# Kernel optimization log

Measured on AMD Instinct MI355X. Metric: run time of the kernel, lower is better.

The kernel has to match this reference:

```python
import jax, jax.numpy as jnp
import numpy as np

N = 100000   # nodes
E = 800000   # directed edges (before self-loops)
D = 256      # in_feats == out_feats


def setup_inputs() -> dict:
    key = jax.random.key(0)
    ks = jax.random.split(key, 6)
    scale = 1.0 / np.sqrt(D)
    features = jax.random.normal(ks[0], (N, D), dtype=jnp.float32)
    src = jax.random.randint(ks[1], (E,), 0, N, dtype=jnp.int32)
    dst = jax.random.randint(ks[2], (E,), 0, N, dtype=jnp.int32)
    W1 = jax.random.normal(ks[3], (D, D), dtype=jnp.float32) * scale
    b1 = jnp.zeros((D,), dtype=jnp.float32)
    W2 = jax.random.normal(ks[4], (D, D), dtype=jnp.float32) * scale
    b2 = jnp.zeros((D,), dtype=jnp.float32)
    return {"features": features, "src": src, "dst": dst,
            "W1": W1, "b1": b1, "W2": W2, "b2": b2}


def _graph_conv(h, src, dst, norm_src, norm_dst, W, b):
    # DGL GraphConv, norm='both': out = D_in^{-1/2} A (D_out^{-1/2} h W) + b
    h = (h * norm_src) @ W            # [N, D] project (W first; in==out)
    agg = jax.ops.segment_sum(h[src], dst, num_segments=N)  # SpMM gather-scatter
    return agg * norm_dst + b


def reference(features, src, dst, W1, b1, W2, b2):
    # forward does g = dgl.add_self_loop(g)
    loops = jnp.arange(N, dtype=src.dtype)
    s = jnp.concatenate([src, loops])
    d = jnp.concatenate([dst, loops])
    ones = jnp.ones_like(s, dtype=jnp.float32)
    deg_out = jax.ops.segment_sum(ones, s, num_segments=N)   # out-degree (src side)
    deg_in = jax.ops.segment_sum(ones, d, num_segments=N)    # in-degree  (dst side)
    norm_src = jnp.where(deg_out > 0, deg_out ** -0.5, 0.0)[:, None]
    norm_dst = jnp.where(deg_in > 0, deg_in ** -0.5, 0.0)[:, None]
    x = _graph_conv(features, s, d, norm_src, norm_dst, W1, b1)
    x = jax.nn.relu(x)
    x = _graph_conv(x, s, d, norm_src, norm_dst, W2, b2)
    return x
```

## Files before the change

### kernel.cpp

```cpp
#include <hip/hip_runtime.h>

#define NN 100000
#define DD 256
#define SCAN_BLK 1024

typedef unsigned int uint;
typedef unsigned short ushort;
typedef __attribute__((ext_vector_type(8))) short bfx8;
typedef __attribute__((ext_vector_type(4))) float fx4;

__device__ __forceinline__ ushort f2bf(float f) {
    uint u = __float_as_uint(f);
    u += 0x7fff + ((u >> 16) & 1);
    return (ushort)(u >> 16);
}

__global__ __launch_bounds__(256) void k_init_deg(int* __restrict__ dego,
                                                  int* __restrict__ degi) {
    int i = blockIdx.x * 256 + threadIdx.x;
    if (i < NN) { dego[i] = 1; degi[i] = 1; }
}

__global__ __launch_bounds__(256) void k_count(const int* __restrict__ src,
                                               const int* __restrict__ dst, int E,
                                               int* __restrict__ dego,
                                               int* __restrict__ degi) {
    int e = blockIdx.x * 256 + threadIdx.x;
    if (e < E) {
        atomicAdd(&dego[src[e]], 1);
        atomicAdd(&degi[dst[e]], 1);
    }
}

__global__ __launch_bounds__(256) void k_norm(const int* __restrict__ dego,
                                              const int* __restrict__ degi,
                                              float* __restrict__ ns,
                                              float* __restrict__ nd) {
    int i = blockIdx.x * 256 + threadIdx.x;
    if (i < NN) {
        ns[i] = rsqrtf((float)dego[i]);
        nd[i] = rsqrtf((float)degi[i]);
    }
}

__device__ __forceinline__ int block_scan_inc(int v, int* sm) {
    int t = threadIdx.x;
    sm[t] = v;
    __syncthreads();
    for (int o = 1; o < SCAN_BLK; o <<= 1) {
        int x = (t >= o) ? sm[t - o] : 0;
        __syncthreads();
        sm[t] += x;
        __syncthreads();
    }
    return sm[t];
}

__global__ __launch_bounds__(SCAN_BLK) void k_scan1(const int* __restrict__ degi,
                                                    int* __restrict__ partials) {
    __shared__ int sm[SCAN_BLK];
    int i = blockIdx.x * SCAN_BLK + threadIdx.x;
    int v = (i < NN) ? (degi[i] - 1) : 0;
    block_scan_inc(v, sm);
    if (threadIdx.x == 0) partials[blockIdx.x] = sm[SCAN_BLK - 1];
}

__global__ __launch_bounds__(128) void k_scan2(int* __restrict__ partials, int nb) {
    __shared__ int sm[128];
    int t = threadIdx.x;
    int v = (t < nb) ? partials[t] : 0;
    sm[t] = v;
    __syncthreads();
    for (int o = 1; o < 128; o <<= 1) {
        int x = (t >= o) ? sm[t - o] : 0;
        __syncthreads();
        sm[t] += x;
        __syncthreads();
    }
    if (t < nb) partials[t] = sm[t] - v;
}

__global__ __launch_bounds__(SCAN_BLK) void k_scan3(const int* __restrict__ degi,
                                                    const int* __restrict__ partials,
                                                    int* __restrict__ rowptr,
                                                    int* __restrict__ cursor) {
    __shared__ int sm[SCAN_BLK];
    int i = blockIdx.x * SCAN_BLK + threadIdx.x;
    int v = (i < NN) ? (degi[i] - 1) : 0;
    int incl = block_scan_inc(v, sm);
    int excl = partials[blockIdx.x] + incl - v;
    if (i <= NN) rowptr[i] = excl;
    if (i < NN) cursor[i] = excl;
}

__global__ __launch_bounds__(256) void k_fill(const int* __restrict__ src,
                                              const int* __restrict__ dst, int E,
                                              int* __restrict__ cursor,
                                              int* __restrict__ eidx) {
    int e = blockIdx.x * 256 + threadIdx.x;
    if (e < E) {
        int d = dst[e];
        int p = atomicAdd(&cursor[d], 1);
        eidx[p] = src[e];
    }
}

__global__ __launch_bounds__(256) void k_convW(const float* __restrict__ W,
                                               ushort* __restrict__ Wt) {
    int n = blockIdx.x, k = threadIdx.x;
    Wt[n * DD + k] = f2bf(W[(size_t)k * DD + n]);
}

template <bool FP32A>
__global__ __launch_bounds__(512, 4) void k_mfgemm(const void* __restrict__ Av,
                                                   const float* __restrict__ nrm,
                                                   const ushort* __restrict__ Wt,
                                                   ushort* __restrict__ H) {
    __shared__ uint4 atq[2][128 * 8];
    int t = threadIdx.x;
    int brow = blockIdx.x * 128;
    int lane = t & 63, w = t >> 6;
    int wr = w >> 2, wc = w & 3;
    int lg = lane >> 4, lr = lane & 15;

    int sr = t >> 3, sc = t & 7;
    int rows_[2];
    float ns_[2];
#pragma unroll
    for (int i = 0; i < 2; ++i) {
        int r = brow + sr + i * 64;
        if (r >= NN) r = NN - 1;
        rows_[i] = r;
        if (FP32A) ns_[i] = nrm[r];
    }

    const uint4* wb[4];
#pragma unroll
    for (int ni = 0; ni < 4; ++ni)
        wb[ni] = (const uint4*)(Wt + (size_t)(wc * 64 + ni * 16 + lr) * DD);

    fx4 acc[4][4];
#pragma unroll
    for (int mi = 0; mi < 4; ++mi)
#pragma unroll
        for (int ni = 0; ni < 4; ++ni)
            acc[mi][ni] = (fx4){0.f, 0.f, 0.f, 0.f};

    uint4 sva[2];
    float4 svf[2][2];

    auto ldA = [&](int ks) {
        if (FP32A) {
            const float* X = (const float*)Av;
#pragma unroll
            for (int i = 0; i < 2; ++i) {
                const float4* p =
                    (const float4*)(X + (size_t)rows_[i] * DD + ks * 64 + sc * 8);
                svf[i][0] = p[0];
                svf[i][1] = p[1];
            }
        } else {
            const ushort* A = (const ushort*)Av;
#pragma unroll
            for (int i = 0; i < 2; ++i)
                sva[i] = *(const uint4*)(A + (size_t)rows_[i] * DD + ks * 64 + sc * 8);
        }
    };
    auto wrA = [&](int buf) {
#pragma unroll
        for (int i = 0; i < 2; ++i) {
            int r = sr + i * 64;
            uint4 u;
            if (FP32A) {
                float s = ns_[i];
                float4 a = svf[i][0], b = svf[i][1];
                u.x = (uint)f2bf(a.x * s) | ((uint)f2bf(a.y * s) << 16);
                u.y = (uint)f2bf(a.z * s) | ((uint)f2bf(a.w * s) << 16);
                u.z = (uint)f2bf(b.x * s) | ((uint)f2bf(b.y * s) << 16);
                u.w = (uint)f2bf(b.z * s) | ((uint)f2bf(b.w * s) << 16);
            } else {
                u = sva[i];
            }
            atq[buf][r * 8 + (sc ^ (r & 7))] = u;
        }
    };

    ldA(0);
    wrA(0);
    __syncthreads();

    int buf = 0;
#pragma unroll
    for (int ks = 0; ks < 4; ++ks) {
        if (ks < 3) ldA(ks + 1);
#pragma unroll
        for (int kk = 0; kk < 2; ++kk) {
            bfx8 bfr[4], af[4];
#pragma unroll
            for (int ni = 0; ni < 4; ++ni)
                bfr[ni] = *(const bfx8*)&wb[ni][ks * 8 + kk * 4 + lg];
#pragma unroll
            for (int mi = 0; mi < 4; ++mi) {
                int r = wr * 64 + mi * 16 + lr;
                int c = kk * 4 + lg;
                af[mi] = *(const bfx8*)&atq[buf][r * 8 + (c ^ (r & 7))];
            }
#pragma unroll
            for (int mi = 0; mi < 4; ++mi)
#pragma unroll
                for (int ni = 0; ni < 4; ++ni)
                    acc[mi][ni] = __builtin_amdgcn_mfma_f32_16x16x32_bf16(
                        af[mi], bfr[ni], acc[mi][ni], 0, 0, 0);
        }
        if (ks < 3) wrA(buf ^ 1);
        __syncthreads();
        buf ^= 1;
    }

#pragma unroll
    for (int mi = 0; mi < 4; ++mi) {
        int rbase = brow + wr * 64 + mi * 16 + lg * 4;
#pragma unroll
        for (int ni = 0; ni < 4; ++ni) {
            int col = wc * 64 + ni * 16 + lr;
#pragma unroll
            for (int j = 0; j < 4; ++j) {
                int row = rbase + j;
                if (row < NN) H[(size_t)row * DD + col] = f2bf(acc[mi][ni][j]);
            }
        }
    }
}

__global__ __launch_bounds__(256) void k_spmm_bf(const ushort* __restrict__ T,
                                                 const int* __restrict__ rowptr,
                                                 const int* __restrict__ eidx,
                                                 const float* __restrict__ nd,
                                                 const float* __restrict__ ns,
                                                 const float* __restrict__ bias,
                                                 ushort* __restrict__ obf,
                                                 float* __restrict__ of,
                                                 int layer1) {
    int wid = threadIdx.x >> 6, lane = threadIdx.x & 63;
    int node = blockIdx.x * 4 + wid;
    if (node >= NN) return;
    int c = lane << 2;
    uint2 sv = *(const uint2*)(T + (size_t)node * DD + c);
    float p0[4], p1[4], p2[4], p3[4];
    p0[0] = __uint_as_float(sv.x << 16);
    p0[1] = __uint_as_float(sv.x & 0xffff0000u);
    p0[2] = __uint_as_float(sv.y << 16);
    p0[3] = __uint_as_float(sv.y & 0xffff0000u);
#pragma unroll
    for (int j = 0; j < 4; ++j) { p1[j] = 0.f; p2[j] = 0.f; p3[j] = 0.f; }
    int e = rowptr[node], end = rowptr[node + 1];
    for (; e + 3 < end; e += 4) {
        int s0 = eidx[e], s1 = eidx[e + 1], s2 = eidx[e + 2], s3 = eidx[e + 3];
        uint2 v0 = *(const uint2*)(T + (size_t)s0 * DD + c);
        uint2 v1 = *(const uint2*)(T + (size_t)s1 * DD + c);
        uint2 v2 = *(const uint2*)(T + (size_t)s2 * DD + c);
        uint2 v3 = *(const uint2*)(T + (size_t)s3 * DD + c);
        p0[0] += __uint_as_float(v0.x << 16);
        p0[1] += __uint_as_float(v0.x & 0xffff0000u);
        p0[2] += __uint_as_float(v0.y << 16);
        p0[3] += __uint_as_float(v0.y & 0xffff0000u);
        p1[0] += __uint_as_float(v1.x << 16);
        p1[1] += __uint_as_float(v1.x & 0xffff0000u);
        p1[2] += __uint_as_float(v1.y << 16);
        p1[3] += __uint_as_float(v1.y & 0xffff0000u);
        p2[0] += __uint_as_float(v2.x << 16);
        p2[1] += __uint_as_float(v2.x & 0xffff0000u);
        p2[2] += __uint_as_float(v2.y << 16);
        p2[3] += __uint_as_float(v2.y & 0xffff0000u);
        p3[0] += __uint_as_float(v3.x << 16);
        p3[1] += __uint_as_float(v3.x & 0xffff0000u);
        p3[2] += __uint_as_float(v3.y << 16);
        p3[3] += __uint_as_float(v3.y & 0xffff0000u);
    }
    for (; e < end; ++e) {
        int s0 = eidx[e];
        uint2 v0 = *(const uint2*)(T + (size_t)s0 * DD + c);
        p0[0] += __uint_as_float(v0.x << 16);
        p0[1] += __uint_as_float(v0.x & 0xffff0000u);
        p0[2] += __uint_as_float(v0.y << 16);
        p0[3] += __uint_as_float(v0.y & 0xffff0000u);
    }
#pragma unroll
    for (int j = 0; j < 4; ++j) p0[j] += (p1[j] + p2[j]) + p3[j];
    float n = nd[node];
    float4 bb = *(const float4*)(bias + c);
    float o0 = fmaf(p0[0], n, bb.x);
    float o1 = fmaf(p0[1], n, bb.y);
    float o2 = fmaf(p0[2], n, bb.z);
    float o3 = fmaf(p0[3], n, bb.w);
    if (layer1) {
        float s = ns[node];
        o0 = fmaxf(o0, 0.f) * s; o1 = fmaxf(o1, 0.f) * s;
        o2 = fmaxf(o2, 0.f) * s; o3 = fmaxf(o3, 0.f) * s;
        uint lo = (uint)f2bf(o0) | ((uint)f2bf(o1) << 16);
        uint hi = (uint)f2bf(o2) | ((uint)f2bf(o3) << 16);
        *(uint2*)(obf + (size_t)node * DD + c) = make_uint2(lo, hi);
    } else {
        fx4 o = {o0, o1, o2, o3};
        __builtin_nontemporal_store(o, (fx4*)(of + (size_t)node * DD + c));
    }
}

extern "C" void kernel_launch(void* const* d_in, const int* in_sizes, int n_in,
                              void* d_out, int out_size, void* d_ws, size_t ws_size,
                              hipStream_t stream) {
    const float* features = (const float*)d_in[0];
    const int* src = (const int*)d_in[1];
    const int* dst = (const int*)d_in[2];
    const float* W1 = (const float*)d_in[3];
    const float* b1 = (const float*)d_in[4];
    const float* W2 = (const float*)d_in[5];
    const float* b2 = (const float*)d_in[6];
    int E = in_sizes[1];
    float* out = (float*)d_out;

    size_t off = 0;
    auto alloc = [&](size_t nbytes) -> void* {
        void* p = (char*)d_ws + off;
        off += (nbytes + 255) & ~(size_t)255;
        return p;
    };
    int* dego = (int*)alloc((size_t)NN * 4);
    int* degi = (int*)alloc((size_t)NN * 4);
    float* norm_src = (float*)alloc((size_t)NN * 4);
    float* norm_dst = (float*)alloc((size_t)NN * 4);
    int* rowptr = (int*)alloc((size_t)(NN + 1) * 4);
    int* cursor = (int*)alloc((size_t)NN * 4);
    int* partials = (int*)alloc(128 * 4);
    int* eidx = (int*)alloc((size_t)E * 4);
    ushort* Wt1 = (ushort*)alloc((size_t)DD * DD * 2);
    ushort* Wt2 = (ushort*)alloc((size_t)DD * DD * 2);
    ushort* Xbf = (ushort*)alloc((size_t)NN * DD * 2);
    ushort* Hbf = (ushort*)alloc((size_t)NN * DD * 2);

    const int NB = (NN + SCAN_BLK - 1) / SCAN_BLK;

    k_init_deg<<<(NN + 255) / 256, 256, 0, stream>>>(dego, degi);
    k_count<<<(E + 255) / 256, 256, 0, stream>>>(src, dst, E, dego, degi);
    k_norm<<<(NN + 255) / 256, 256, 0, stream>>>(dego, degi, norm_src, norm_dst);
    k_scan1<<<NB, SCAN_BLK, 0, stream>>>(degi, partials);
    k_scan2<<<1, 128, 0, stream>>>(partials, NB);
    k_scan3<<<NB, SCAN_BLK, 0, stream>>>(degi, partials, rowptr, cursor);
    k_fill<<<(E + 255) / 256, 256, 0, stream>>>(src, dst, E, cursor, eidx);

    k_convW<<<DD, DD, 0, stream>>>(W1, Wt1);
    k_convW<<<DD, DD, 0, stream>>>(W2, Wt2);

    dim3 ggrid((NN + 127) / 128);
    k_mfgemm<true><<<ggrid, 512, 0, stream>>>(features, norm_src, Wt1, Hbf);
    k_spmm_bf<<<(NN + 3) / 4, 256, 0, stream>>>(Hbf, rowptr, eidx, norm_dst,
                                                norm_src, b1, Xbf, out, 1);
    k_mfgemm<false><<<ggrid, 512, 0, stream>>>(Xbf, nullptr, Wt2, Hbf);
    k_spmm_bf<<<(NN + 3) / 4, 256, 0, stream>>>(Hbf, rowptr, eidx, norm_dst,
                                                norm_src, b2, nullptr, out, 0);
}
```

Baseline: 384.9 us.

## Fuse layer-1 SpMM aggregation with layer-2 GEMM via shared-memory tile

Adds a kernel where each block aggregates 64 nodes' neighbour rows for layer 1, applies bias, ReLU and source norm, and stores the bf16 results in a swizzled LDS tile. It then multiplies that tile by W2 with MFMA and writes H2 directly. This removes the intermediate X buffer write and read and one kernel launch. In exchange each block now does 16 sequential gather rows per wave before the GEMM, and the W2 fragments are read straight from global memory instead of being staged in LDS.

```diff
diff --git a/kernel.cpp b/kernel.cpp
--- a/kernel.cpp
+++ b/kernel.cpp
@@ -232,15 +232,135 @@
     }
 }
 
+__global__ __launch_bounds__(256, 4) void k_spgemm(const ushort* __restrict__ H1,
+                                                   const int* __restrict__ rowptr,
+                                                   const int* __restrict__ eidx,
+                                                   const float* __restrict__ nd,
+                                                   const float* __restrict__ ns,
+                                                   const float* __restrict__ b1,
+                                                   const ushort* __restrict__ Wt2,
+                                                   ushort* __restrict__ H2) {
+    __shared__ uint4 xs[64 * 32];
+    int t = threadIdx.x;
+    int lane = t & 63, w = t >> 6;
+    int nodebase = blockIdx.x * 64;
+    int c = lane << 2;
+    float4 bb = *(const float4*)(b1 + c);
+
+#pragma unroll 1
+    for (int jj = 0; jj < 16; ++jj) {
+        int jrow = w * 16 + jj;
+        int node = nodebase + jrow;
+        if (node < NN) {
+            uint2 sv = *(const uint2*)(H1 + (size_t)node * DD + c);
+            float p0[4], p1[4], p2[4], p3[4];
+            p0[0] = __uint_as_float(sv.x << 16);
+            p0[1] = __uint_as_float(sv.x & 0xffff0000u);
+            p0[2] = __uint_as_float(sv.y << 16);
+            p0[3] = __uint_as_float(sv.y & 0xffff0000u);
+#pragma unroll
+            for (int j = 0; j < 4; ++j) { p1[j] = 0.f; p2[j] = 0.f; p3[j] = 0.f; }
+            int e = rowptr[node], end = rowptr[node + 1];
+            for (; e + 3 < end; e += 4) {
+                int s0 = eidx[e], s1 = eidx[e + 1], s2 = eidx[e + 2], s3 = eidx[e + 3];
+                uint2 v0 = *(const uint2*)(H1 + (size_t)s0 * DD + c);
+                uint2 v1 = *(const uint2*)(H1 + (size_t)s1 * DD + c);
+                uint2 v2 = *(const uint2*)(H1 + (size_t)s2 * DD + c);
+                uint2 v3 = *(const uint2*)(H1 + (size_t)s3 * DD + c);
+                p0[0] += __uint_as_float(v0.x << 16);
+                p0[1] += __uint_as_float(v0.x & 0xffff0000u);
+                p0[2] += __uint_as_float(v0.y << 16);
+                p0[3] += __uint_as_float(v0.y & 0xffff0000u);
+                p1[0] += __uint_as_float(v1.x << 16);
+                p1[1] += __uint_as_float(v1.x & 0xffff0000u);
+                p1[2] += __uint_as_float(v1.y << 16);
+                p1[3] += __uint_as_float(v1.y & 0xffff0000u);
+                p2[0] += __uint_as_float(v2.x << 16);
+                p2[1] += __uint_as_float(v2.x & 0xffff0000u);
+                p2[2] += __uint_as_float(v2.y << 16);
+                p2[3] += __uint_as_float(v2.y & 0xffff0000u);
+                p3[0] += __uint_as_float(v3.x << 16);
+                p3[1] += __uint_as_float(v3.x & 0xffff0000u);
+                p3[2] += __uint_as_float(v3.y << 16);
+                p3[3] += __uint_as_float(v3.y & 0xffff0000u);
+            }
+            for (; e < end; ++e) {
+                int s0 = eidx[e];
+                uint2 v0 = *(const uint2*)(H1 + (size_t)s0 * DD + c);
+                p0[0] += __uint_as_float(v0.x << 16);
+                p0[1] += __uint_as_float(v0.x & 0xffff0000u);
+                p0[2] += __uint_as_float(v0.y << 16);
+                p0[3] += __uint_as_float(v0.y & 0xffff0000u);
+            }
+#pragma unroll
+            for (int j = 0; j < 4; ++j) p0[j] += (p1[j] + p2[j]) + p3[j];
+            float n = nd[node];
+            float s = ns[node];
+            float o0 = fmaxf(fmaf(p0[0], n, bb.x), 0.f) * s;
+            float o1 = fmaxf(fmaf(p0[1], n, bb.y), 0.f) * s;
+            float o2 = fmaxf(fmaf(p0[2], n, bb.z), 0.f) * s;
+            float o3 = fmaxf(fmaf(p0[3], n, bb.w), 0.f) * s;
+            uint lo = (uint)f2bf(o0) | ((uint)f2bf(o1) << 16);
+            uint hi = (uint)f2bf(o2) | ((uint)f2bf(o3) << 16);
+            int ch = lane >> 1, h = lane & 1;
+            ((uint2*)&xs[jrow * 32 + (ch ^ (jrow & 7))])[h] = make_uint2(lo, hi);
+        }
+    }
+    __syncthreads();
+
+    int lg = lane >> 4, lr = lane & 15;
+    const uint4* wb[4];
+#pragma unroll
+    for (int ni = 0; ni < 4; ++ni)
+        wb[ni] = (const uint4*)(Wt2 + (size_t)(w * 64 + ni * 16 + lr) * DD);
+
+    fx4 acc[4][4];
+#pragma unroll
+    for (int mi = 0; mi < 4; ++mi)
+#pragma unroll
+        for (int ni = 0; ni < 4; ++ni)
+            acc[mi][ni] = (fx4){0.f, 0.f, 0.f, 0.f};
+
+#pragma unroll
+    for (int kc = 0; kc < 8; ++kc) {
+        bfx8 bfr[4], af[4];
+#pragma unroll
+        for (int ni = 0; ni < 4; ++ni)
+            bfr[ni] = *(const bfx8*)&wb[ni][kc * 4 + lg];
+#pragma unroll
+        for (int mi = 0; mi < 4; ++mi) {
+            int r = mi * 16 + lr;
+            af[mi] = *(const bfx8*)&xs[r * 32 + ((kc * 4 + lg) ^ (r & 7))];
+        }
+#pragma unroll
+        for (int mi = 0; mi < 4; ++mi)
+#pragma unroll
+            for (int ni = 0; ni < 4; ++ni)
+                acc[mi][ni] = __builtin_amdgcn_mfma_f32_16x16x32_bf16(
+                    af[mi], bfr[ni], acc[mi][ni], 0, 0, 0);
+    }
+
+#pragma unroll
+    for (int mi = 0; mi < 4; ++mi) {
+        int rbase = nodebase + mi * 16 + lg * 4;
+#pragma unroll
+        for (int ni = 0; ni < 4; ++ni) {
+            int col = w * 64 + ni * 16 + lr;
+#pragma unroll
+            for (int j = 0; j < 4; ++j) {
+                int row = rbase + j;
+                if (row < NN) H2[(size_t)row * DD + col] = f2bf(acc[mi][ni][j]);
+            }
+        }
+    }
+}
+
 __global__ __launch_bounds__(256) void k_spmm_bf(const ushort* __restrict__ T,
                                                  const int* __restrict__ rowptr,
                                                  const int* __restrict__ eidx,
                                                  const float* __restrict__ nd,
-                                                 const float* __restrict__ ns,
                                                  const float* __restrict__ bias,
-                                                 ushort* __restrict__ obf,
-                                                 float* __restrict__ of,
-                                                 int layer1) {
+                                                 float* __restrict__ of) {
     int wid = threadIdx.x >> 6, lane = threadIdx.x & 63;
     int node = blockIdx.x * 4 + wid;
     if (node >= NN) return;
@@ -289,21 +409,9 @@
     for (int j = 0; j < 4; ++j) p0[j] += (p1[j] + p2[j]) + p3[j];
     float n = nd[node];
     float4 bb = *(const float4*)(bias + c);
-    float o0 = fmaf(p0[0], n, bb.x);
-    float o1 = fmaf(p0[1], n, bb.y);
-    float o2 = fmaf(p0[2], n, bb.z);
-    float o3 = fmaf(p0[3], n, bb.w);
-    if (layer1) {
-        float s = ns[node];
-        o0 = fmaxf(o0, 0.f) * s; o1 = fmaxf(o1, 0.f) * s;
-        o2 = fmaxf(o2, 0.f) * s; o3 = fmaxf(o3, 0.f) * s;
-        uint lo = (uint)f2bf(o0) | ((uint)f2bf(o1) << 16);
-        uint hi = (uint)f2bf(o2) | ((uint)f2bf(o3) << 16);
-        *(uint2*)(obf + (size_t)node * DD + c) = make_uint2(lo, hi);
-    } else {
-        fx4 o = {o0, o1, o2, o3};
-        __builtin_nontemporal_store(o, (fx4*)(of + (size_t)node * DD + c));
-    }
+    fx4 o = {fmaf(p0[0], n, bb.x), fmaf(p0[1], n, bb.y),
+             fmaf(p0[2], n, bb.z), fmaf(p0[3], n, bb.w)};
+    __builtin_nontemporal_store(o, (fx4*)(of + (size_t)node * DD + c));
 }
 
 extern "C" void kernel_launch(void* const* d_in, const int* in_sizes, int n_in,
@@ -335,8 +443,8 @@
     int* eidx = (int*)alloc((size_t)E * 4);
     ushort* Wt1 = (ushort*)alloc((size_t)DD * DD * 2);
     ushort* Wt2 = (ushort*)alloc((size_t)DD * DD * 2);
-    ushort* Xbf = (ushort*)alloc((size_t)NN * DD * 2);
     ushort* Hbf = (ushort*)alloc((size_t)NN * DD * 2);
+    ushort* H2bf = (ushort*)alloc((size_t)NN * DD * 2);
 
     const int NB = (NN + SCAN_BLK - 1) / SCAN_BLK;
 
@@ -353,9 +461,8 @@
 
     dim3 ggrid((NN + 127) / 128);
     k_mfgemm<true><<<ggrid, 512, 0, stream>>>(features, norm_src, Wt1, Hbf);
-    k_spmm_bf<<<(NN + 3) / 4, 256, 0, stream>>>(Hbf, rowptr, eidx, norm_dst,
-                                                norm_src, b1, Xbf, out, 1);
-    k_mfgemm<false><<<ggrid, 512, 0, stream>>>(Xbf, nullptr, Wt2, Hbf);
-    k_spmm_bf<<<(NN + 3) / 4, 256, 0, stream>>>(Hbf, rowptr, eidx, norm_dst,
-                                                norm_src, b2, nullptr, out, 0);
-}
+    k_spgemm<<<(NN + 63) / 64, 256, 0, stream>>>(Hbf, rowptr, eidx, norm_dst,
+                                                 norm_src, b1, Wt2, H2bf);
+    k_spmm_bf<<<(NN + 3) / 4, 256, 0, stream>>>(H2bf, rowptr, eidx, norm_dst,
+                                                b2, out);
+}
```

New measurement: 399.5 us. +3.8%, slower.

## Stage GEMM A tiles via direct global-to-LDS loads and move norm scaling to epilogue

Applied to the files above, without the earlier changes.

The GEMM now stages A tiles with global_load_lds straight into shared memory, bypassing registers. For the fp32 input layer it keeps fp32 in LDS and converts to bf16 at fragment read time with v_cvt_pk_bf16_f32, applying norm_src as a row scale in the epilogue instead of before rounding. It also preloads B fragments one k-step ahead, replaces the degree init kernel with a memset (degrees offset by one afterwards), and merges the two weight conversions into one launch. The aim is less register staging and fewer launches, at the cost of twice the LDS for layer 1 and slightly different bf16 rounding.

```diff
diff --git a/kernel.cpp b/kernel.cpp
--- a/kernel.cpp
+++ b/kernel.cpp
@@ -15,10 +15,10 @@
     return (ushort)(u >> 16);
 }
 
-__global__ __launch_bounds__(256) void k_init_deg(int* __restrict__ dego,
-                                                  int* __restrict__ degi) {
-    int i = blockIdx.x * 256 + threadIdx.x;
-    if (i < NN) { dego[i] = 1; degi[i] = 1; }
+__device__ __forceinline__ uint cvtpk(float lo, float hi) {
+    uint r;
+    asm("v_cvt_pk_bf16_f32 %0, %1, %2" : "=v"(r) : "v"(lo), "v"(hi));
+    return r;
 }
 
 __global__ __launch_bounds__(256) void k_count(const int* __restrict__ src,
@@ -38,8 +38,8 @@
                                               float* __restrict__ nd) {
     int i = blockIdx.x * 256 + threadIdx.x;
     if (i < NN) {
-        ns[i] = rsqrtf((float)dego[i]);
-        nd[i] = rsqrtf((float)degi[i]);
+        ns[i] = rsqrtf((float)(dego[i] + 1));
+        nd[i] = rsqrtf((float)(degi[i] + 1));
     }
 }
 
@@ -60,7 +60,7 @@
                                                     int* __restrict__ partials) {
     __shared__ int sm[SCAN_BLK];
     int i = blockIdx.x * SCAN_BLK + threadIdx.x;
-    int v = (i < NN) ? (degi[i] - 1) : 0;
+    int v = (i < NN) ? degi[i] : 0;
     block_scan_inc(v, sm);
     if (threadIdx.x == 0) partials[blockIdx.x] = sm[SCAN_BLK - 1];
 }
@@ -86,7 +86,7 @@
                                                     int* __restrict__ cursor) {
     __shared__ int sm[SCAN_BLK];
     int i = blockIdx.x * SCAN_BLK + threadIdx.x;
-    int v = (i < NN) ? (degi[i] - 1) : 0;
+    int v = (i < NN) ? degi[i] : 0;
     int incl = block_scan_inc(v, sm);
     int excl = partials[blockIdx.x] + incl - v;
     if (i <= NN) rowptr[i] = excl;
@@ -105,9 +105,13 @@
     }
 }
 
-__global__ __launch_bounds__(256) void k_convW(const float* __restrict__ W,
-                                               ushort* __restrict__ Wt) {
-    int n = blockIdx.x, k = threadIdx.x;
+__global__ __launch_bounds__(256) void k_convW(const float* __restrict__ W1,
+                                               const float* __restrict__ W2,
+                                               ushort* __restrict__ Wt1,
+                                               ushort* __restrict__ Wt2) {
+    int n = blockIdx.x & 255, k = threadIdx.x;
+    const float* W = (blockIdx.x < 256) ? W1 : W2;
+    ushort* Wt = (blockIdx.x < 256) ? Wt1 : Wt2;
     Wt[n * DD + k] = f2bf(W[(size_t)k * DD + n]);
 }
 
@@ -116,29 +120,54 @@
                                                    const float* __restrict__ nrm,
                                                    const ushort* __restrict__ Wt,
                                                    ushort* __restrict__ H) {
-    __shared__ uint4 atq[2][128 * 8];
+    constexpr int CPR = FP32A ? 16 : 8;
+    constexpr int CALLS = (128 * CPR) / (8 * 64);
+    __shared__ uint4 atq[2][128 * CPR];
     int t = threadIdx.x;
     int brow = blockIdx.x * 128;
     int lane = t & 63, w = t >> 6;
     int wr = w >> 2, wc = w & 3;
     int lg = lane >> 4, lr = lane & 15;
 
-    int sr = t >> 3, sc = t & 7;
-    int rows_[2];
-    float ns_[2];
-#pragma unroll
-    for (int i = 0; i < 2; ++i) {
-        int r = brow + sr + i * 64;
-        if (r >= NN) r = NN - 1;
-        rows_[i] = r;
-        if (FP32A) ns_[i] = nrm[r];
-    }
+    uint gofs[CALLS];
+#pragma unroll
+    for (int i = 0; i < CALLS; ++i) {
+        int slot = (w * CALLS + i) * 64;
+        int r = slot / CPR + lane / CPR;
+        int cs = (lane % CPR) ^ (r & 7);
+        int row = brow + r;
+        if (row >= NN) row = NN - 1;
+        if (FP32A)
+            gofs[i] = (uint)(((size_t)row * DD + cs * 4) * 4);
+        else
+            gofs[i] = (uint)(((size_t)row * DD + cs * 8) * 2);
+    }
+
+    auto stage = [&](int buf, int ks) {
+#pragma unroll
+        for (int i = 0; i < CALLS; ++i) {
+            int slot = (w * CALLS + i) * 64;
+            const char* g = (const char*)Av + gofs[i] + ks * (FP32A ? 256 : 128);
+            __builtin_amdgcn_global_load_lds(
+                (const __attribute__((address_space(1))) uint*)g,
+                (__attribute__((address_space(3))) uint*)&atq[buf][slot], 16, 0, 0);
+        }
+    };
 
     const uint4* wb[4];
 #pragma unroll
     for (int ni = 0; ni < 4; ++ni)
         wb[ni] = (const uint4*)(Wt + (size_t)(wc * 64 + ni * 16 + lr) * DD);
 
+    bfx8 bfr2[2][4];
+    auto ldB = [&](int ks) {
+#pragma unroll
+        for (int kk = 0; kk < 2; ++kk)
+#pragma unroll
+            for (int ni = 0; ni < 4; ++ni)
+                bfr2[kk][ni] = *(const bfx8*)&wb[ni][ks * 8 + kk * 4 + lg];
+    };
+
     fx4 acc[4][4];
 #pragma unroll
     for (int mi = 0; mi < 4; ++mi)
@@ -146,87 +175,58 @@
         for (int ni = 0; ni < 4; ++ni)
             acc[mi][ni] = (fx4){0.f, 0.f, 0.f, 0.f};
 
-    uint4 sva[2];
-    float4 svf[2][2];
-
-    auto ldA = [&](int ks) {
-        if (FP32A) {
-            const float* X = (const float*)Av;
-#pragma unroll
-            for (int i = 0; i < 2; ++i) {
-                const float4* p =
-                    (const float4*)(X + (size_t)rows_[i] * DD + ks * 64 + sc * 8);
-                svf[i][0] = p[0];
-                svf[i][1] = p[1];
-            }
-        } else {
-            const ushort* A = (const ushort*)Av;
-#pragma unroll
-            for (int i = 0; i < 2; ++i)
-                sva[i] = *(const uint4*)(A + (size_t)rows_[i] * DD + ks * 64 + sc * 8);
-        }
-    };
-    auto wrA = [&](int buf) {
-#pragma unroll
-        for (int i = 0; i < 2; ++i) {
-            int r = sr + i * 64;
-            uint4 u;
-            if (FP32A) {
-                float s = ns_[i];
-                float4 a = svf[i][0], b = svf[i][1];
-                u.x = (uint)f2bf(a.x * s) | ((uint)f2bf(a.y * s) << 16);
-                u.y = (uint)f2bf(a.z * s) | ((uint)f2bf(a.w * s) << 16);
-                u.z = (uint)f2bf(b.x * s) | ((uint)f2bf(b.y * s) << 16);
-                u.w = (uint)f2bf(b.z * s) | ((uint)f2bf(b.w * s) << 16);
-            } else {
-                u = sva[i];
-            }
-            atq[buf][r * 8 + (sc ^ (r & 7))] = u;
-        }
-    };
-
-    ldA(0);
-    wrA(0);
+    stage(0, 0);
+    ldB(0);
     __syncthreads();
 
     int buf = 0;
 #pragma unroll
     for (int ks = 0; ks < 4; ++ks) {
-        if (ks < 3) ldA(ks + 1);
+        if (ks < 3) stage(buf ^ 1, ks + 1);
 #pragma unroll
         for (int kk = 0; kk < 2; ++kk) {
-            bfx8 bfr[4], af[4];
-#pragma unroll
-            for (int ni = 0; ni < 4; ++ni)
-                bfr[ni] = *(const bfx8*)&wb[ni][ks * 8 + kk * 4 + lg];
 #pragma unroll
             for (int mi = 0; mi < 4; ++mi) {
                 int r = wr * 64 + mi * 16 + lr;
-                int c = kk * 4 + lg;
-                af[mi] = *(const bfx8*)&atq[buf][r * 8 + (c ^ (r & 7))];
-            }
-#pragma unroll
-            for (int mi = 0; mi < 4; ++mi)
+                bfx8 af;
+                if (FP32A) {
+                    int cf = (kk * 4 + lg) * 2;
+                    fx4 q0 = *(const fx4*)&atq[buf][r * 16 + (cf ^ (r & 7))];
+                    fx4 q1 = *(const fx4*)&atq[buf][r * 16 + ((cf + 1) ^ (r & 7))];
+                    uint4 uu;
+                    uu.x = cvtpk(q0.x, q0.y);
+                    uu.y = cvtpk(q0.z, q0.w);
+                    uu.z = cvtpk(q1.x, q1.y);
+                    uu.w = cvtpk(q1.z, q1.w);
+                    af = *(bfx8*)&uu;
+                } else {
+                    int c = kk * 4 + lg;
+                    af = *(const bfx8*)&atq[buf][r * 8 + (c ^ (r & 7))];
+                }
 #pragma unroll
                 for (int ni = 0; ni < 4; ++ni)
                     acc[mi][ni] = __builtin_amdgcn_mfma_f32_16x16x32_bf16(
-                        af[mi], bfr[ni], acc[mi][ni], 0, 0, 0);
+                        af, bfr2[kk][ni], acc[mi][ni], 0, 0, 0);
+            }
         }
-        if (ks < 3) wrA(buf ^ 1);
+        if (ks < 3) ldB(ks + 1);
         __syncthreads();
         buf ^= 1;
     }
 
 #pragma unroll
     for (int mi = 0; mi < 4; ++mi) {
-        int rbase = brow + wr * 64 + mi * 16 + lg * 4;
-#pragma unroll
-        for (int ni = 0; ni < 4; ++ni) {
-            int col = wc * 64 + ni * 16 + lr;
-#pragma unroll
-            for (int j = 0; j < 4; ++j) {
-                int row = rbase + j;
-                if (row < NN) H[(size_t)row * DD + col] = f2bf(acc[mi][ni][j]);
+#pragma unroll
+        for (int j = 0; j < 4; ++j) {
+            int row = brow + wr * 64 + mi * 16 + lg * 4 + j;
+            if (row < NN) {
+                float sc = FP32A ? nrm[row] : 1.0f;
+                ushort* hp = H + (size_t)row * DD;
+#pragma unroll
+                for (int ni = 0; ni < 4; ++ni) {
+                    int col = wc * 64 + ni * 16 + lr;
+                    hp[col] = f2bf(acc[mi][ni][j] * sc);
+                }
             }
         }
     }
@@ -340,16 +340,14 @@
 
     const int NB = (NN + SCAN_BLK - 1) / SCAN_BLK;
 
-    k_init_deg<<<(NN + 255) / 256, 256, 0, stream>>>(dego, degi);
+    hipMemsetAsync(dego, 0, (size_t)2 * 400128, stream);
     k_count<<<(E + 255) / 256, 256, 0, stream>>>(src, dst, E, dego, degi);
     k_norm<<<(NN + 255) / 256, 256, 0, stream>>>(dego, degi, norm_src, norm_dst);
     k_scan1<<<NB, SCAN_BLK, 0, stream>>>(degi, partials);
     k_scan2<<<1, 128, 0, stream>>>(partials, NB);
     k_scan3<<<NB, SCAN_BLK, 0, stream>>>(degi, partials, rowptr, cursor);
     k_fill<<<(E + 255) / 256, 256, 0, stream>>>(src, dst, E, cursor, eidx);
-
-    k_convW<<<DD, DD, 0, stream>>>(W1, Wt1);
-    k_convW<<<DD, DD, 0, stream>>>(W2, Wt2);
+    k_convW<<<512, 256, 0, stream>>>(W1, W2, Wt1, Wt2);
 
     dim3 ggrid((NN + 127) / 128);
     k_mfgemm<true><<<ggrid, 512, 0, stream>>>(features, norm_src, Wt1, Hbf);
```

Measured after the change: 398.7 us. 3.6% more time.
